# Optimization experiments

Measured on AMD Instinct MI355X. Metric: run time of the kernel, lower is better.

## Reference

```python
import jax, jax.numpy as jnp
import numpy as np

B, S, D, H, W = 2, 4096, 1024, 8, 1024  # batch, seq, model_dim, heads, window
DH = D // H
EPS = 1e-5


def setup_inputs() -> dict:
    key = jax.random.key(0)
    ks = jax.random.split(key, 4)
    scale = 0.02
    return {
        "val": jax.random.normal(ks[0], (B, S, D), dtype=jnp.float32),
        "w_qkv": jax.random.normal(ks[1], (D, 3 * D), dtype=jnp.float32) * scale,
        "b_qkv": jnp.zeros((3 * D,), dtype=jnp.float32),
        "w_out": jax.random.normal(ks[2], (D, D), dtype=jnp.float32) * scale,
        "b_out": jnp.zeros((D,), dtype=jnp.float32),
        "ln_gamma": jnp.ones((D,), dtype=jnp.float32),
        "ln_beta": jnp.zeros((D,), dtype=jnp.float32),
    }


def _layer_norm(x, gamma, beta):
    mu = jnp.mean(x, axis=-1, keepdims=True)
    var = jnp.mean(jnp.square(x - mu), axis=-1, keepdims=True)
    return (x - mu) * jax.lax.rsqrt(var + EPS) * gamma + beta


def reference(val, w_qkv, b_qkv, w_out, b_out, ln_gamma, ln_beta):
    nb = S // W  # number of local windows
    qkv = val @ w_qkv + b_qkv                       # [B, S, 3D]
    qkv = qkv.reshape(B, nb, W, 3, H, DH)
    q, k, v = qkv[..., 0, :, :], qkv[..., 1, :, :], qkv[..., 2, :, :]  # [B,nb,W,H,DH]
    scores = jnp.einsum("bnwhd,bnxhd->bnhwx", q, k) / jnp.sqrt(jnp.float32(DH))
    attn = jax.nn.softmax(scores, axis=-1)          # [B,nb,H,W,W]
    ctx = jnp.einsum("bnhwx,bnxhd->bnwhd", attn, v).reshape(B, S, D)
    attn_out = ctx @ w_out + b_out                  # [B,S,D]
    return _layer_norm(val + attn_out, ln_gamma, ln_beta)
```

## Files before the change

### kernel.cpp

```cpp
#include <hip/hip_runtime.h>
#include <hip/hip_bf16.h>
#include <stdint.h>


typedef float f32x4 __attribute__((ext_vector_type(4)));
typedef __bf16 bf16x8 __attribute__((ext_vector_type(8)));

static __device__ __forceinline__ unsigned short f2bf(float f) {
    unsigned int u = __builtin_bit_cast(unsigned int, f);
    u += 0x7fffu + ((u >> 16) & 1u);
    return (unsigned short)(u >> 16);
}

static __device__ __forceinline__ unsigned cvt_pk_bf16(float lo, float hi) {
    unsigned r;
    asm("v_cvt_pk_bf16_f32 %0, %1, %2" : "=v"(r) : "v"(lo), "v"(hi));
    return r;
}

static __device__ __forceinline__ void gload_lds16(const void* g, void* l) {
    __builtin_amdgcn_global_load_lds(
        (__attribute__((address_space(1))) void*)(g),
        (__attribute__((address_space(3))) void*)(l), 16, 0, 0);
}

#define VMCNT(n) asm volatile("s_waitcnt vmcnt(" #n ")" ::: "memory")
#define SB() __builtin_amdgcn_sched_barrier(0)

__global__ __launch_bounds__(256) void k_convert(const float* __restrict__ in,
                                                 unsigned short* __restrict__ out,
                                                 int n4) {
    int i = blockIdx.x * 256 + threadIdx.x;
    if (i >= n4) return;
    float4 v = ((const float4*)in)[i];
    ushort4 o;
    o.x = f2bf(v.x); o.y = f2bf(v.y); o.z = f2bf(v.z); o.w = f2bf(v.w);
    ((ushort4*)out)[i] = o;
}

__global__ __launch_bounds__(256) void k_transpose(const float* __restrict__ in,
                                                   unsigned short* __restrict__ out,
                                                   int R, int C) {
    __shared__ float tile[64][65];
    const int rt = blockIdx.y * 64, ct = blockIdx.x * 64;
    const int t = threadIdx.x;
#pragma unroll
    for (int i = 0; i < 4; ++i) {
        int fid = i * 256 + t;
        int r = fid >> 4;
        int c = (fid & 15) << 2;
        float4 v = *(const float4*)&in[(size_t)(rt + r) * C + ct + c];
        tile[r][c] = v.x; tile[r][c + 1] = v.y; tile[r][c + 2] = v.z; tile[r][c + 3] = v.w;
    }
    __syncthreads();
#pragma unroll
    for (int i = 0; i < 4; ++i) {
        int fid = i * 256 + t;
        int c = fid >> 4;
        int r0 = (fid & 15) << 2;
        ushort4 o;
        o.x = f2bf(tile[r0][c]);     o.y = f2bf(tile[r0 + 1][c]);
        o.z = f2bf(tile[r0 + 2][c]); o.w = f2bf(tile[r0 + 3][c]);
        *(ushort4*)&out[(size_t)(ct + c) * R + rt + r0] = o;
    }
}

__global__ __launch_bounds__(512, 1) void k_gemm1(
    const unsigned short* __restrict__ A,
    const unsigned short* __restrict__ Bt,
    const float* __restrict__ bias,
    unsigned short* __restrict__ out_qk,
    unsigned short* __restrict__ out_vT)
{
    __shared__ __align__(16) char smem[131072];
    const int t = threadIdx.x;
    const int wave = t >> 6, lane = t & 63;
    const int lr = lane & 15, lg = lane >> 4;
    const int wr = wave >> 2, wc = wave & 3;

    const int lid = blockIdx.x;
    const int swz = (lid & 7) * 48 + (lid >> 3);
    const int tile_m = (swz / 12) * 256;
    const int tile_n = (swz % 12) * 256;

    const int srow8 = lane >> 3;
    const int sblk = (lane & 7) ^ srow8;

    f32x4 acc[8][4];
#pragma unroll
    for (int i = 0; i < 8; ++i)
#pragma unroll
        for (int j = 0; j < 4; ++j)
            acc[i][j] = (f32x4){0.f, 0.f, 0.f, 0.f};

    auto stage2 = [&](int kt, int buf, int h) {
#pragma unroll
        for (int i = 0; i < 2; ++i) {
            int r = i * 64 + wave * 8 + srow8;
            int dst = buf * 32768 + h * 16384 + (i * 512 + wave * 64) * 16;
            gload_lds16(&A[(size_t)(tile_m + h * 128 + r) * 1024 + kt * 64 + sblk * 8],
                        smem + dst);
            gload_lds16(&Bt[(size_t)(tile_n + h * 128 + r) * 1024 + kt * 64 + sblk * 8],
                        smem + 65536 + dst);
        }
    };

    stage2(0, 0, 0);
    stage2(0, 0, 1);
    VMCNT(0);
    SB(); __builtin_amdgcn_s_barrier(); SB();

    bf16x8 af[4][2], bf0[2][2], bf1[2][2];

    for (int tt = 0; tt < 8; ++tt) {
#pragma unroll
        for (int p = 0; p < 8; ++p) {
            const int b = p >> 2, q = p & 3;
            const int mh = q >> 1, nh = q & 1;
            const int abase = b * 32768;
            const int bbase = 65536 + b * 32768;
            if (nh == 0) {
#pragma unroll
                for (int mi = 0; mi < 4; ++mi) {
                    const int row = wr * 128 + mh * 64 + mi * 16 + lr;
#pragma unroll
                    for (int kk = 0; kk < 2; ++kk)
                        af[mi][kk] = *(const bf16x8*)(smem + abase + row * 128 +
                                        (((kk * 4 + lg) ^ (row & 7)) << 4));
                }
            }
            if (q == 0) {
#pragma unroll
                for (int ni = 0; ni < 2; ++ni) {
                    const int row = wc * 64 + ni * 16 + lr;
#pragma unroll
                    for (int kk = 0; kk < 2; ++kk)
                        bf0[ni][kk] = *(const bf16x8*)(smem + bbase + row * 128 +
                                        (((kk * 4 + lg) ^ (row & 7)) << 4));
                }
            }
            if (q == 1) {
#pragma unroll
                for (int ni = 0; ni < 2; ++ni) {
                    const int row = wc * 64 + 32 + ni * 16 + lr;
#pragma unroll
                    for (int kk = 0; kk < 2; ++kk)
                        bf1[ni][kk] = *(const bf16x8*)(smem + bbase + row * 128 +
                                        (((kk * 4 + lg) ^ (row & 7)) << 4));
                }
            }
            if (p == 0) stage2(2 * tt + 1, 1, 0);
            if (p == 1) stage2(2 * tt + 1, 1, 1);
            if (p == 4 && tt < 7) stage2(2 * tt + 2, 0, 0);
            if (p == 5 && tt < 7) stage2(2 * tt + 2, 0, 1);

            SB(); __builtin_amdgcn_s_barrier(); SB();

            __builtin_amdgcn_s_setprio(1);
#pragma unroll
            for (int kk = 0; kk < 2; ++kk)
#pragma unroll
                for (int mi = 0; mi < 4; ++mi)
#pragma unroll
                    for (int ni = 0; ni < 2; ++ni) {
                        if (nh == 0)
                            acc[mh * 4 + mi][ni] = __builtin_amdgcn_mfma_f32_16x16x32_bf16(
                                af[mi][kk], bf0[ni][kk], acc[mh * 4 + mi][ni], 0, 0, 0);
                        else
                            acc[mh * 4 + mi][2 + ni] = __builtin_amdgcn_mfma_f32_16x16x32_bf16(
                                af[mi][kk], bf1[ni][kk], acc[mh * 4 + mi][2 + ni], 0, 0, 0);
                    }
            __builtin_amdgcn_s_setprio(0);

            if (q == 3) { VMCNT(0); }
            SB(); __builtin_amdgcn_s_barrier(); SB();
        }
    }

#pragma unroll
    for (int J = 0; J < 4; ++J) {
        const int n = tile_n + wc * 64 + (J >> 1) * 32 + (J & 1) * 16 + lr;
        const float bv = bias[n];
#pragma unroll
        for (int I = 0; I < 8; ++I) {
            const int m0 = tile_m + wr * 128 + (I >> 2) * 64 + (I & 3) * 16 + lg * 4;
            f32x4 v = acc[I][J];
            if (n < 2048) {
#pragma unroll
                for (int r = 0; r < 4; ++r)
                    out_qk[(size_t)(m0 + r) * 2048 + n] = f2bf(v[r] + bv);
            } else {
                int hd = (n - 2048) >> 7;
                int dd = (n - 2048) & 127;
                int bn = m0 >> 10;
                int x0 = m0 & 1023;
                ushort4 o;
                o.x = f2bf(v[0] + bv); o.y = f2bf(v[1] + bv);
                o.z = f2bf(v[2] + bv); o.w = f2bf(v[3] + bv);
                *(ushort4*)&out_vT[((size_t)(bn * 8 + hd) * 128 + dd) * 1024 + x0] = o;
            }
        }
    }
}

__global__ __launch_bounds__(256, 2) void k_gemm2(
    const unsigned short* __restrict__ A,
    const unsigned short* __restrict__ Bt,
    const float* __restrict__ bias,
    const float* __restrict__ resid,
    float* __restrict__ out_f,
    int Kdim)
{
    __shared__ __align__(16) unsigned short Al[128 * 64];
    __shared__ __align__(16) unsigned short Bl[128 * 64];
    const int t = threadIdx.x;
    const int wave = t >> 6, lane = t & 63;
    const int wm = wave >> 1, wn = wave & 1;
    const int lr = lane & 15, lg = lane >> 4;
    const int tile_m = blockIdx.y * 128;
    const int tile_n = blockIdx.x * 128;

    f32x4 acc[4][4];
#pragma unroll
    for (int i = 0; i < 4; ++i)
#pragma unroll
        for (int j = 0; j < 4; ++j)
            acc[i][j] = (f32x4){0.f, 0.f, 0.f, 0.f};

    const int srow = lane >> 3;
    const int scol = (lane & 7) * 8;

    for (int kt = 0; kt < Kdim; kt += 64) {
#pragma unroll
        for (int i = 0; i < 4; ++i) {
            int chunk = i * 4 + wave;
            int row = chunk * 8 + srow;
            gload_lds16(&A[(size_t)(tile_m + row) * Kdim + kt + scol], &Al[chunk * 512]);
            gload_lds16(&Bt[(size_t)(tile_n + row) * Kdim + kt + scol], &Bl[chunk * 512]);
        }
        __syncthreads();
#pragma unroll
        for (int kk = 0; kk < 2; ++kk) {
            bf16x8 af[4], bfr[4];
#pragma unroll
            for (int mi = 0; mi < 4; ++mi)
                af[mi] = *(const bf16x8*)&Al[(wm * 64 + mi * 16 + lr) * 64 + kk * 32 + lg * 8];
#pragma unroll
            for (int ni = 0; ni < 4; ++ni)
                bfr[ni] = *(const bf16x8*)&Bl[(wn * 64 + ni * 16 + lr) * 64 + kk * 32 + lg * 8];
#pragma unroll
            for (int mi = 0; mi < 4; ++mi)
#pragma unroll
                for (int ni = 0; ni < 4; ++ni)
                    acc[mi][ni] = __builtin_amdgcn_mfma_f32_16x16x32_bf16(af[mi], bfr[ni], acc[mi][ni], 0, 0, 0);
        }
        __syncthreads();
    }

#pragma unroll
    for (int ni = 0; ni < 4; ++ni) {
        int n = tile_n + wn * 64 + ni * 16 + lr;
        float bv = bias[n];
#pragma unroll
        for (int mi = 0; mi < 4; ++mi) {
            int m0 = tile_m + wm * 64 + mi * 16 + lg * 4;
            f32x4 v = acc[mi][ni];
#pragma unroll
            for (int r = 0; r < 4; ++r) {
                size_t idx = (size_t)(m0 + r) * 1024 + n;
                out_f[idx] = v[r] + bv + resid[idx];
            }
        }
    }
}

__global__ __launch_bounds__(256, 2) void k_attn(
    const unsigned short* __restrict__ qk,
    const unsigned short* __restrict__ vT,
    unsigned short* __restrict__ ctx)
{
    __shared__ __align__(16) unsigned short Kl[2 * 64 * 128];
    __shared__ __align__(16) unsigned short Vl[2 * 128 * 64];
    __shared__ __align__(16) unsigned short Pl[128 * 64];
    const int t = threadIdx.x;
    const int wave = t >> 6, lane = t & 63;
    const int lr = lane & 15, lg = lane >> 4;

    const int lid = blockIdx.y * gridDim.x + blockIdx.x;
    const int xcd = lid & 7, slot = lid >> 3;
    const int head = xcd * 8 + (slot & 7);
    const int qblk = slot >> 3;

    const int h = head & 7;
    const int tok0 = (head >> 3) * 1024;
    const int qtok = tok0 + qblk * 128 + wave * 32;
    const float cl2 = 0.08838834764831845f * 1.44269504088896f;

    const unsigned short* kbase = &qk[(size_t)tok0 * 2048 + 1024 + h * 128];
    const unsigned short* vhead = &vT[(size_t)head * 128 * 1024];

    auto stage = [&](int x0, int buf) {
        unsigned short* Kb = (unsigned short*)((char*)Kl + buf * 16384);
        unsigned short* Vb = (unsigned short*)((char*)Vl + buf * 16384);
#pragma unroll
        for (int i = 0; i < 4; ++i) {
            int x = i * 16 + wave * 4 + (lane >> 4);
            int ck = (lane & 15) ^ (x & 7);
            gload_lds16(&kbase[(size_t)(x0 + x) * 2048 + ck * 8], &Kb[i * 2048 + wave * 512]);
            int d = i * 32 + wave * 8 + (lane >> 3);
            int cv = (lane & 7) ^ (d & 7);
            gload_lds16(&vhead[(size_t)d * 1024 + x0 + cv * 8], &Vb[i * 2048 + wave * 512]);
        }
    };

    bf16x8 qf[2][4];
#pragma unroll
    for (int nq = 0; nq < 2; ++nq)
#pragma unroll
        for (int kk = 0; kk < 4; ++kk)
            qf[nq][kk] = *(const bf16x8*)&qk[(size_t)(qtok + 16 * nq + lr) * 2048 + h * 128 + kk * 32 + lg * 8];

    f32x4 o[2][8];
#pragma unroll
    for (int a = 0; a < 2; ++a)
#pragma unroll
        for (int b = 0; b < 8; ++b)
            o[a][b] = (f32x4){0.f, 0.f, 0.f, 0.f};
    float m_run[2] = {-3.0e38f, -3.0e38f};
    float l_run[2] = {0.f, 0.f};

    stage(0, 0);

    for (int tile = 0; tile < 16; ++tile) {
        const int kb = (tile & 1) * 16384;
        if (tile < 15) {
            stage((tile + 1) * 64, (tile + 1) & 1);
            VMCNT(8);
        } else {
            VMCNT(0);
        }
        SB(); __builtin_amdgcn_s_barrier(); SB();

        f32x4 s[4][2];
#pragma unroll
        for (int mi = 0; mi < 4; ++mi)
#pragma unroll
            for (int nq = 0; nq < 2; ++nq)
                s[mi][nq] = (f32x4){0.f, 0.f, 0.f, 0.f};
#pragma unroll
        for (int kk = 0; kk < 4; ++kk) {
            bf16x8 kf[4];
#pragma unroll
            for (int mi = 0; mi < 4; ++mi) {
                int row = mi * 16 + lr;
                int byte = (row * 256 + kk * 64 + lg * 16) ^ ((row & 7) << 4);
                kf[mi] = *(const bf16x8*)((const char*)Kl + kb + byte);
            }
            __builtin_amdgcn_s_setprio(1);
#pragma unroll
            for (int mi = 0; mi < 4; ++mi)
#pragma unroll
                for (int nq = 0; nq < 2; ++nq)
                    s[mi][nq] = __builtin_amdgcn_mfma_f32_16x16x32_bf16(kf[mi], qf[nq][kk], s[mi][nq], 0, 0, 0);
            __builtin_amdgcn_s_setprio(0);
        }

        float fac[2];
        bool doresc[2];
#pragma unroll
        for (int nq = 0; nq < 2; ++nq) {
            float mx = -3.0e38f;
#pragma unroll
            for (int mi = 0; mi < 4; ++mi)
#pragma unroll
                for (int r = 0; r < 4; ++r)
                    mx = fmaxf(mx, s[mi][nq][r]);
            mx = fmaxf(mx, __shfl_xor(mx, 16));
            mx = fmaxf(mx, __shfl_xor(mx, 32));
            float mxl = mx * cl2;
            float mr = m_run[nq];
            if (__any(mxl - mr > 8.0f)) {
                float mn = fmaxf(mr, mxl);
                fac[nq] = __builtin_amdgcn_exp2f(mr - mn);
                m_run[nq] = mn;
                doresc[nq] = true;
            } else {
                fac[nq] = 1.0f;
                doresc[nq] = false;
            }
            const float nmn = -m_run[nq];
            float sum = 0.f;
            const int q = wave * 32 + nq * 16 + lr;
#pragma unroll
            for (int mi = 0; mi < 4; ++mi) {
                float p0 = __builtin_amdgcn_exp2f(__builtin_fmaf(s[mi][nq][0], cl2, nmn));
                float p1 = __builtin_amdgcn_exp2f(__builtin_fmaf(s[mi][nq][1], cl2, nmn));
                float p2 = __builtin_amdgcn_exp2f(__builtin_fmaf(s[mi][nq][2], cl2, nmn));
                float p3 = __builtin_amdgcn_exp2f(__builtin_fmaf(s[mi][nq][3], cl2, nmn));
                sum += (p0 + p1) + (p2 + p3);
                uint2 pk;
                pk.x = cvt_pk_bf16(p0, p1);
                pk.y = cvt_pk_bf16(p2, p3);
                int byte = (q * 128 + (mi * 16 + lg * 4) * 2) ^ ((q & 7) << 4);
                *(uint2*)((char*)Pl + byte) = pk;
            }
            sum += __shfl_xor(sum, 16);
            sum += __shfl_xor(sum, 32);
            l_run[nq] = l_run[nq] * fac[nq] + sum;
        }

#pragma unroll
        for (int mo = 0; mo < 2; ++mo)
            if (doresc[mo]) {
#pragma unroll
                for (int r = 0; r < 4; ++r) {
                    int src = (lane & 48) | (lg * 4 + r);
                    float f = __shfl(fac[mo], src);
#pragma unroll
                    for (int nd = 0; nd < 8; ++nd)
                        o[mo][nd][r] *= f;
                }
            }

#pragma unroll
        for (int kk = 0; kk < 2; ++kk) {
            bf16x8 pf[2], vf[8];
#pragma unroll
            for (int mo = 0; mo < 2; ++mo) {
                int q = wave * 32 + mo * 16 + lr;
                int byte = (q * 128 + kk * 64 + lg * 16) ^ ((q & 7) << 4);
                pf[mo] = *(const bf16x8*)((const char*)Pl + byte);
            }
#pragma unroll
            for (int nd = 0; nd < 8; ++nd) {
                int drow = nd * 16 + lr;
                int byte = (drow * 128 + kk * 64 + lg * 16) ^ ((drow & 7) << 4);
                vf[nd] = *(const bf16x8*)((const char*)Vl + kb + byte);
            }
            __builtin_amdgcn_s_setprio(1);
#pragma unroll
            for (int mo = 0; mo < 2; ++mo)
#pragma unroll
                for (int nd = 0; nd < 8; ++nd)
                    o[mo][nd] = __builtin_amdgcn_mfma_f32_16x16x32_bf16(pf[mo], vf[nd], o[mo][nd], 0, 0, 0);
            __builtin_amdgcn_s_setprio(0);
        }
        __builtin_amdgcn_s_barrier(); SB();
    }

#pragma unroll
    for (int mo = 0; mo < 2; ++mo) {
        float rl[4];
#pragma unroll
        for (int r = 0; r < 4; ++r) {
            int src = (lane & 48) | (lg * 4 + r);
            rl[r] = 1.0f / __shfl(l_run[mo], src);
        }
#pragma unroll
        for (int nd = 0; nd < 8; ++nd)
#pragma unroll
            for (int r = 0; r < 4; ++r) {
                int q = qtok + mo * 16 + lg * 4 + r;
                ctx[(size_t)q * 1024 + h * 128 + nd * 16 + lr] = f2bf(o[mo][nd][r] * rl[r]);
            }
    }
}

__global__ __launch_bounds__(256) void k_ln(float* __restrict__ io,
                                            const float* __restrict__ gamma,
                                            const float* __restrict__ beta)
{
    __shared__ float bs[4], bss[4];
    const int row = blockIdx.x;
    const int t = threadIdx.x;
    float4 v = ((const float4*)&io[(size_t)row * 1024])[t];
    float s = (v.x + v.y) + (v.z + v.w);
    float ss = (v.x * v.x + v.y * v.y) + (v.z * v.z + v.w * v.w);
#pragma unroll
    for (int off = 32; off >= 1; off >>= 1) {
        s += __shfl_xor(s, off);
        ss += __shfl_xor(ss, off);
    }
    if ((t & 63) == 0) { bs[t >> 6] = s; bss[t >> 6] = ss; }
    __syncthreads();
    s = (bs[0] + bs[1]) + (bs[2] + bs[3]);
    ss = (bss[0] + bss[1]) + (bss[2] + bss[3]);
    const float mu = s * (1.f / 1024.f);
    const float var = ss * (1.f / 1024.f) - mu * mu;
    const float rs = rsqrtf(var + 1e-5f);
    float4 g = ((const float4*)gamma)[t];
    float4 b = ((const float4*)beta)[t];
    float4 ov;
    ov.x = (v.x - mu) * rs * g.x + b.x;
    ov.y = (v.y - mu) * rs * g.y + b.y;
    ov.z = (v.z - mu) * rs * g.z + b.z;
    ov.w = (v.w - mu) * rs * g.w + b.w;
    ((float4*)&io[(size_t)row * 1024])[t] = ov;
}

extern "C" void kernel_launch(void* const* d_in, const int* in_sizes, int n_in,
                              void* d_out, int out_size, void* d_ws, size_t ws_size,
                              hipStream_t stream)
{
    const float* val   = (const float*)d_in[0];
    const float* w_qkv = (const float*)d_in[1];
    const float* b_qkv = (const float*)d_in[2];
    const float* w_out = (const float*)d_in[3];
    const float* b_out = (const float*)d_in[4];
    const float* ln_g  = (const float*)d_in[5];
    const float* ln_b  = (const float*)d_in[6];
    float* out = (float*)d_out;

    char* ws = (char*)d_ws;
    unsigned short* qk     = (unsigned short*)(ws + 0);
    unsigned short* vTb    = (unsigned short*)(ws + 33554432);
    unsigned short* ctx    = (unsigned short*)(ws + 50331648);
    unsigned short* w_outT = (unsigned short*)(ws + 67108864);
    unsigned short* w_qkvT = (unsigned short*)(ws + 69206016);
    unsigned short* valb   = (unsigned short*)(ws + 75497472);

    k_convert<<<8192, 256, 0, stream>>>(val, valb, 2097152);
    k_transpose<<<dim3(48, 16), 256, 0, stream>>>(w_qkv, w_qkvT, 1024, 3072);
    k_transpose<<<dim3(16, 16), 256, 0, stream>>>(w_out, w_outT, 1024, 1024);
    k_gemm1<<<384, 512, 0, stream>>>(valb, w_qkvT, b_qkv, qk, vTb);
    k_attn<<<dim3(8, 64), 256, 0, stream>>>(qk, vTb, ctx);
    k_gemm2<<<dim3(8, 64), 256, 0, stream>>>(ctx, w_outT, b_out, val, out, 1024);
    k_ln<<<8192, 256, 0, stream>>>(out, ln_g, ln_b);
}
```

Measured before the change: 181.4 us.

## Split QKV GEMM tile across 16 waves with smaller per-wave subtiles

Doubles the QKV projection GEMM block from 8 to 16 waves, so each wave owns a 64x64 output subtile instead of 128x64. This halves accumulator and fragment registers per wave and makes each wave stage one row per buffer half instead of two. The intent is more waves in flight to hide LDS and MFMA latency. In exchange, each wave reloads its A and B fragments on every phase, and barriers now sync twice as many waves.

```diff
diff --git a/kernel.cpp b/kernel.cpp
--- a/kernel.cpp
+++ b/kernel.cpp
@@ -65,7 +65,7 @@
     }
 }
 
-__global__ __launch_bounds__(512, 1) void k_gemm1(
+__global__ __launch_bounds__(1024) void k_gemm1(
     const unsigned short* __restrict__ A,
     const unsigned short* __restrict__ Bt,
     const float* __restrict__ bias,
@@ -83,26 +83,23 @@
     const int tile_m = (swz / 12) * 256;
     const int tile_n = (swz % 12) * 256;
 
-    const int srow8 = lane >> 3;
-    const int sblk = (lane & 7) ^ srow8;
-
-    f32x4 acc[8][4];
-#pragma unroll
-    for (int i = 0; i < 8; ++i)
+    const int srow = lane >> 3;
+    const int sblk = (lane & 7) ^ srow;
+
+    f32x4 acc[4][4];
+#pragma unroll
+    for (int i = 0; i < 4; ++i)
 #pragma unroll
         for (int j = 0; j < 4; ++j)
             acc[i][j] = (f32x4){0.f, 0.f, 0.f, 0.f};
 
     auto stage2 = [&](int kt, int buf, int h) {
-#pragma unroll
-        for (int i = 0; i < 2; ++i) {
-            int r = i * 64 + wave * 8 + srow8;
-            int dst = buf * 32768 + h * 16384 + (i * 512 + wave * 64) * 16;
-            gload_lds16(&A[(size_t)(tile_m + h * 128 + r) * 1024 + kt * 64 + sblk * 8],
-                        smem + dst);
-            gload_lds16(&Bt[(size_t)(tile_n + h * 128 + r) * 1024 + kt * 64 + sblk * 8],
-                        smem + 65536 + dst);
-        }
+        const int r = wave * 8 + srow;
+        const int dst = buf * 32768 + h * 16384 + wave * 1024 + lane * 16;
+        gload_lds16(&A[(size_t)(tile_m + h * 128 + r) * 1024 + kt * 64 + sblk * 8],
+                    smem + dst);
+        gload_lds16(&Bt[(size_t)(tile_n + h * 128 + r) * 1024 + kt * 64 + sblk * 8],
+                    smem + 65536 + dst);
     };
 
     stage2(0, 0, 0);
@@ -110,7 +107,7 @@
     VMCNT(0);
     SB(); __builtin_amdgcn_s_barrier(); SB();
 
-    bf16x8 af[4][2], bf0[2][2], bf1[2][2];
+    bf16x8 af[2][2], bf[2][2];
 
     for (int tt = 0; tt < 8; ++tt) {
 #pragma unroll
@@ -119,35 +116,21 @@
             const int mh = q >> 1, nh = q & 1;
             const int abase = b * 32768;
             const int bbase = 65536 + b * 32768;
-            if (nh == 0) {
-#pragma unroll
-                for (int mi = 0; mi < 4; ++mi) {
-                    const int row = wr * 128 + mh * 64 + mi * 16 + lr;
-#pragma unroll
-                    for (int kk = 0; kk < 2; ++kk)
-                        af[mi][kk] = *(const bf16x8*)(smem + abase + row * 128 +
-                                        (((kk * 4 + lg) ^ (row & 7)) << 4));
-                }
-            }
-            if (q == 0) {
-#pragma unroll
-                for (int ni = 0; ni < 2; ++ni) {
-                    const int row = wc * 64 + ni * 16 + lr;
-#pragma unroll
-                    for (int kk = 0; kk < 2; ++kk)
-                        bf0[ni][kk] = *(const bf16x8*)(smem + bbase + row * 128 +
-                                        (((kk * 4 + lg) ^ (row & 7)) << 4));
-                }
-            }
-            if (q == 1) {
-#pragma unroll
-                for (int ni = 0; ni < 2; ++ni) {
-                    const int row = wc * 64 + 32 + ni * 16 + lr;
-#pragma unroll
-                    for (int kk = 0; kk < 2; ++kk)
-                        bf1[ni][kk] = *(const bf16x8*)(smem + bbase + row * 128 +
-                                        (((kk * 4 + lg) ^ (row & 7)) << 4));
-                }
+#pragma unroll
+            for (int mi = 0; mi < 2; ++mi) {
+                const int row = wr * 64 + mh * 32 + mi * 16 + lr;
+#pragma unroll
+                for (int kk = 0; kk < 2; ++kk)
+                    af[mi][kk] = *(const bf16x8*)(smem + abase + row * 128 +
+                                    (((kk * 4 + lg) ^ (row & 7)) << 4));
+            }
+#pragma unroll
+            for (int ni = 0; ni < 2; ++ni) {
+                const int row = wc * 64 + nh * 32 + ni * 16 + lr;
+#pragma unroll
+                for (int kk = 0; kk < 2; ++kk)
+                    bf[ni][kk] = *(const bf16x8*)(smem + bbase + row * 128 +
+                                    (((kk * 4 + lg) ^ (row & 7)) << 4));
             }
             if (p == 0) stage2(2 * tt + 1, 1, 0);
             if (p == 1) stage2(2 * tt + 1, 1, 1);
@@ -160,16 +143,11 @@
 #pragma unroll
             for (int kk = 0; kk < 2; ++kk)
 #pragma unroll
-                for (int mi = 0; mi < 4; ++mi)
-#pragma unroll
-                    for (int ni = 0; ni < 2; ++ni) {
-                        if (nh == 0)
-                            acc[mh * 4 + mi][ni] = __builtin_amdgcn_mfma_f32_16x16x32_bf16(
-                                af[mi][kk], bf0[ni][kk], acc[mh * 4 + mi][ni], 0, 0, 0);
-                        else
-                            acc[mh * 4 + mi][2 + ni] = __builtin_amdgcn_mfma_f32_16x16x32_bf16(
-                                af[mi][kk], bf1[ni][kk], acc[mh * 4 + mi][2 + ni], 0, 0, 0);
-                    }
+                for (int mi = 0; mi < 2; ++mi)
+#pragma unroll
+                    for (int ni = 0; ni < 2; ++ni)
+                        acc[mh * 2 + mi][nh * 2 + ni] = __builtin_amdgcn_mfma_f32_16x16x32_bf16(
+                            af[mi][kk], bf[ni][kk], acc[mh * 2 + mi][nh * 2 + ni], 0, 0, 0);
             __builtin_amdgcn_s_setprio(0);
 
             if (q == 3) { VMCNT(0); }
@@ -182,8 +160,8 @@
         const int n = tile_n + wc * 64 + (J >> 1) * 32 + (J & 1) * 16 + lr;
         const float bv = bias[n];
 #pragma unroll
-        for (int I = 0; I < 8; ++I) {
-            const int m0 = tile_m + wr * 128 + (I >> 2) * 64 + (I & 3) * 16 + lg * 4;
+        for (int I = 0; I < 4; ++I) {
+            const int m0 = tile_m + wr * 64 + (I >> 1) * 32 + (I & 1) * 16 + lg * 4;
             f32x4 v = acc[I][J];
             if (n < 2048) {
 #pragma unroll
@@ -522,7 +500,7 @@
     k_convert<<<8192, 256, 0, stream>>>(val, valb, 2097152);
     k_transpose<<<dim3(48, 16), 256, 0, stream>>>(w_qkv, w_qkvT, 1024, 3072);
     k_transpose<<<dim3(16, 16), 256, 0, stream>>>(w_out, w_outT, 1024, 1024);
-    k_gemm1<<<384, 512, 0, stream>>>(valb, w_qkvT, b_qkv, qk, vTb);
+    k_gemm1<<<384, 1024, 0, stream>>>(valb, w_qkvT, b_qkv, qk, vTb);
     k_attn<<<dim3(8, 64), 256, 0, stream>>>(qk, vTb, ctx);
     k_gemm2<<<dim3(8, 64), 256, 0, stream>>>(ctx, w_outT, b_out, val, out, 1024);
     k_ln<<<8192, 256, 0, stream>>>(out, ln_g, ln_b);
```

Measured after the change: 220.3 us. 1.21x slower.

## Restructure output GEMM with 256x128 tiles, triple-buffered LDS pipeline and swizzle

Applied to the files above, without the earlier changes.

The output projection GEMM moves from 128x128 tiles with 256 threads and single-buffered synchronous loads to 256x128 tiles with 512 threads. It uses a three-stage LDS ring filled by async global-to-LDS loads, XOR-swizzled LDS layout to avoid bank conflicts, and vmcnt-based waits. Loads are split into half-stages interleaved with MFMA bursts under raised priority, and a blockIdx swizzle improves L2 locality. The gemm1 launch bounds also change to request two waves per EU. The aim is to hide memory latency and increase operand reuse, at the cost of large LDS use and fewer blocks.

```diff
diff --git a/kernel.cpp b/kernel.cpp
--- a/kernel.cpp
+++ b/kernel.cpp
@@ -65,7 +65,9 @@
     }
 }
 
-__global__ __launch_bounds__(512, 1) void k_gemm1(
+__global__ __launch_bounds__(512)
+__attribute__((amdgpu_waves_per_eu(2, 2)))
+void k_gemm1(
     const unsigned short* __restrict__ A,
     const unsigned short* __restrict__ Bt,
     const float* __restrict__ bias,
@@ -203,22 +205,26 @@
     }
 }
 
-__global__ __launch_bounds__(256, 2) void k_gemm2(
+__global__ __launch_bounds__(512) void k_gemm2(
     const unsigned short* __restrict__ A,
     const unsigned short* __restrict__ Bt,
     const float* __restrict__ bias,
     const float* __restrict__ resid,
-    float* __restrict__ out_f,
-    int Kdim)
+    float* __restrict__ out_f)
 {
-    __shared__ __align__(16) unsigned short Al[128 * 64];
-    __shared__ __align__(16) unsigned short Bl[128 * 64];
+    __shared__ __align__(16) char smem[147456];
     const int t = threadIdx.x;
     const int wave = t >> 6, lane = t & 63;
-    const int wm = wave >> 1, wn = wave & 1;
     const int lr = lane & 15, lg = lane >> 4;
-    const int tile_m = blockIdx.y * 128;
-    const int tile_n = blockIdx.x * 128;
+    const int wr = wave >> 1, wc = wave & 1;
+
+    const int lid = blockIdx.x;
+    const int swz = (lid & 7) * 32 + (lid >> 3);
+    const int tile_m = (swz / 8) * 256;
+    const int tile_n = (swz % 8) * 128;
+
+    const int srow = lane >> 3;
+    const int sblk = (lane & 7) ^ srow;
 
     f32x4 acc[4][4];
 #pragma unroll
@@ -227,44 +233,90 @@
         for (int j = 0; j < 4; ++j)
             acc[i][j] = (f32x4){0.f, 0.f, 0.f, 0.f};
 
-    const int srow = lane >> 3;
-    const int scol = (lane & 7) * 8;
-
-    for (int kt = 0; kt < Kdim; kt += 64) {
-#pragma unroll
-        for (int i = 0; i < 4; ++i) {
-            int chunk = i * 4 + wave;
-            int row = chunk * 8 + srow;
-            gload_lds16(&A[(size_t)(tile_m + row) * Kdim + kt + scol], &Al[chunk * 512]);
-            gload_lds16(&Bt[(size_t)(tile_n + row) * Kdim + kt + scol], &Bl[chunk * 512]);
-        }
-        __syncthreads();
-#pragma unroll
-        for (int kk = 0; kk < 2; ++kk) {
-            bf16x8 af[4], bfr[4];
+    auto stage2 = [&](int kt, int buf, int h) {
+#pragma unroll
+        for (int i = 0; i < 2; ++i) {
+            int r = h * 128 + i * 64 + wave * 8 + srow;
+            int dst = buf * 49152 + h * 16384 + i * 8192 + wave * 1024 + lane * 16;
+            gload_lds16(&A[(size_t)(tile_m + r) * 1024 + kt * 64 + sblk * 8], smem + dst);
+        }
+        int rb = h * 64 + wave * 8 + srow;
+        int dstb = buf * 49152 + 32768 + h * 8192 + wave * 1024 + lane * 16;
+        gload_lds16(&Bt[(size_t)(tile_n + rb) * 1024 + kt * 64 + sblk * 8], smem + dstb);
+    };
+
+    stage2(0, 0, 0); stage2(0, 0, 1);
+    stage2(1, 1, 0); stage2(1, 1, 1);
+
+    bf16x8 af[4][2], bf[2][2];
+
+    for (int kt = 0; kt < 16; ++kt) {
+        const int buf = kt % 3;
+        if (kt == 15) { VMCNT(0); } else { VMCNT(6); }
+        SB(); __builtin_amdgcn_s_barrier(); SB();
+
+        const int abase = buf * 49152;
+        const int bbase = buf * 49152 + 32768;
+
+#pragma unroll
+        for (int mi = 0; mi < 4; ++mi) {
+            const int row = wr * 64 + mi * 16 + lr;
+#pragma unroll
+            for (int kk = 0; kk < 2; ++kk)
+                af[mi][kk] = *(const bf16x8*)(smem + abase + row * 128 +
+                                (((kk * 4 + lg) ^ (row & 7)) << 4));
+        }
+#pragma unroll
+        for (int ni = 0; ni < 2; ++ni) {
+            const int row = wc * 64 + ni * 16 + lr;
+#pragma unroll
+            for (int kk = 0; kk < 2; ++kk)
+                bf[ni][kk] = *(const bf16x8*)(smem + bbase + row * 128 +
+                                (((kk * 4 + lg) ^ (row & 7)) << 4));
+        }
+        if (kt < 14) stage2(kt + 2, (kt + 2) % 3, 0);
+
+        __builtin_amdgcn_s_setprio(1);
+#pragma unroll
+        for (int kk = 0; kk < 2; ++kk)
 #pragma unroll
             for (int mi = 0; mi < 4; ++mi)
-                af[mi] = *(const bf16x8*)&Al[(wm * 64 + mi * 16 + lr) * 64 + kk * 32 + lg * 8];
-#pragma unroll
-            for (int ni = 0; ni < 4; ++ni)
-                bfr[ni] = *(const bf16x8*)&Bl[(wn * 64 + ni * 16 + lr) * 64 + kk * 32 + lg * 8];
+#pragma unroll
+                for (int ni = 0; ni < 2; ++ni)
+                    acc[mi][ni] = __builtin_amdgcn_mfma_f32_16x16x32_bf16(
+                        af[mi][kk], bf[ni][kk], acc[mi][ni], 0, 0, 0);
+        __builtin_amdgcn_s_setprio(0);
+
+#pragma unroll
+        for (int ni = 0; ni < 2; ++ni) {
+            const int row = wc * 64 + 32 + ni * 16 + lr;
+#pragma unroll
+            for (int kk = 0; kk < 2; ++kk)
+                bf[ni][kk] = *(const bf16x8*)(smem + bbase + row * 128 +
+                                (((kk * 4 + lg) ^ (row & 7)) << 4));
+        }
+        if (kt < 14) stage2(kt + 2, (kt + 2) % 3, 1);
+
+        __builtin_amdgcn_s_setprio(1);
+#pragma unroll
+        for (int kk = 0; kk < 2; ++kk)
 #pragma unroll
             for (int mi = 0; mi < 4; ++mi)
 #pragma unroll
-                for (int ni = 0; ni < 4; ++ni)
-                    acc[mi][ni] = __builtin_amdgcn_mfma_f32_16x16x32_bf16(af[mi], bfr[ni], acc[mi][ni], 0, 0, 0);
-        }
-        __syncthreads();
-    }
-
-#pragma unroll
-    for (int ni = 0; ni < 4; ++ni) {
-        int n = tile_n + wn * 64 + ni * 16 + lr;
-        float bv = bias[n];
-#pragma unroll
-        for (int mi = 0; mi < 4; ++mi) {
-            int m0 = tile_m + wm * 64 + mi * 16 + lg * 4;
-            f32x4 v = acc[mi][ni];
+                for (int ni = 0; ni < 2; ++ni)
+                    acc[mi][2 + ni] = __builtin_amdgcn_mfma_f32_16x16x32_bf16(
+                        af[mi][kk], bf[ni][kk], acc[mi][2 + ni], 0, 0, 0);
+        __builtin_amdgcn_s_setprio(0);
+    }
+
+#pragma unroll
+    for (int J = 0; J < 4; ++J) {
+        const int n = tile_n + wc * 64 + J * 16 + lr;
+        const float bv = bias[n];
+#pragma unroll
+        for (int I = 0; I < 4; ++I) {
+            const int m0 = tile_m + wr * 64 + I * 16 + lg * 4;
+            f32x4 v = acc[I][J];
 #pragma unroll
             for (int r = 0; r < 4; ++r) {
                 size_t idx = (size_t)(m0 + r) * 1024 + n;
@@ -524,6 +576,6 @@
     k_transpose<<<dim3(16, 16), 256, 0, stream>>>(w_out, w_outT, 1024, 1024);
     k_gemm1<<<384, 512, 0, stream>>>(valb, w_qkvT, b_qkv, qk, vTb);
     k_attn<<<dim3(8, 64), 256, 0, stream>>>(qk, vTb, ctx);
-    k_gemm2<<<dim3(8, 64), 256, 0, stream>>>(ctx, w_outT, b_out, val, out, 1024);
+    k_gemm2<<<256, 512, 0, stream>>>(ctx, w_outT, b_out, val, out);
     k_ln<<<8192, 256, 0, stream>>>(out, ln_g, ln_b);
 }
```

Result: faster. 173.6 us (-4.3%).
